# Kernel optimization log

Measured on AMD Instinct MI355X. Metric: run time of the kernel, lower is better.

## Reference

```python
import jax, jax.numpy as jnp
import numpy as np

NUM_HEADS = 16
HEAD_DIM = 64
ROPE_BASE = 10000.0


def _rope_cos_sin(seq_len, head_dim, dtype):
    inv_freq = 1.0 / (ROPE_BASE ** (jnp.arange(0, head_dim, 2, dtype=jnp.float32) / head_dim))
    t = jnp.arange(seq_len, dtype=jnp.float32)
    freqs = t[:, None] * inv_freq[None, :]          # (S, head_dim/2)
    emb = jnp.concatenate([freqs, freqs], axis=-1)  # (S, head_dim)
    return jnp.cos(emb).astype(dtype), jnp.sin(emb).astype(dtype)


def _rotate_half(x):
    x1, x2 = jnp.split(x, 2, axis=-1)
    return jnp.concatenate([-x2, x1], axis=-1)


def setup_inputs() -> dict:
    key = jax.random.key(0)
    k1, k2, k3 = jax.random.split(key, 3)
    B, S, D = 2, 2048, 1024
    x = jax.random.normal(k1, (B, S, D), dtype=jnp.float32)
    Wq = jax.random.normal(k2, (D, D), dtype=jnp.float32) * (D ** -0.5)
    Wkv = jax.random.normal(k3, (2 * D, D), dtype=jnp.float32) * (D ** -0.5)
    mask = jnp.tril(jnp.ones((S, S), dtype=jnp.int32))  # causal mask
    return {"x": x, "Wq": Wq, "Wkv": Wkv, "mask": mask}


def reference(x, Wq, Wkv, mask):
    B, S, D = x.shape
    H, Hd = NUM_HEADS, HEAD_DIM

    # projections (torch Linear: x @ W.T)
    q = (x @ Wq.T).reshape(B, S, H, Hd).transpose(0, 2, 1, 3)           # (B,H,S,Hd)
    kv = (x @ Wkv.T).reshape(B, S, H, Hd, 2).transpose(0, 2, 1, 3, 4)   # (B,H,S,Hd,2)
    k = kv[..., 0]
    v = kv[..., 1]

    # RoPE
    cos, sin = _rope_cos_sin(S, Hd, x.dtype)  # (S,Hd) broadcast over (B,H)
    q = q * cos + _rotate_half(q) * sin
    k = k * cos + _rotate_half(k) * sin

    # attention with full score materialization (faithful to source)
    scale = 1.0 / jnp.sqrt(jnp.asarray(Hd, dtype=x.dtype))
    scores = jnp.einsum('bhqd,bhkd->bhqk', q, k) * scale                # (B,H,S,S)
    scores = jnp.where(mask == 0, -jnp.inf, scores)
    attn = jax.nn.softmax(scores, axis=-1)
    out = jnp.einsum('bhqk,bhkd->bhqd', attn, v)                        # (B,H,S,Hd)
    return out.transpose(0, 2, 1, 3).reshape(B, S, D)
```

## Files before the change

kernel.cpp:

```cpp
#include <hip/hip_runtime.h>
#include <hip/hip_bf16.h>
#include <math.h>


typedef short bfrag __attribute__((ext_vector_type(8)));
typedef float f32x4 __attribute__((ext_vector_type(4)));

__device__ __forceinline__ float bf2f(ushort u) {
    union { uint i; float f; } v; v.i = ((uint)u) << 16; return v.f;
}
__device__ __forceinline__ ushort f2bf(float f) {
    union { uint i; float f; } v; v.f = f;
    uint u = v.i;
    return (ushort)((u + 0x7fffu + ((u >> 16) & 1u)) >> 16);
}

#define MFMA16 __builtin_amdgcn_mfma_f32_16x16x32_bf16

__device__ __forceinline__ void gl_lds16(const ushort* g, ushort* l) {
    __builtin_amdgcn_global_load_lds(
        (const __attribute__((address_space(1))) void*)g,
        (__attribute__((address_space(3))) void*)l, 16, 0, 0);
}

__global__ __launch_bounds__(256)
void cvt_bf16(const float* __restrict__ x, const float* __restrict__ wq,
              const float* __restrict__ wkv, ushort* __restrict__ xb,
              ushort* __restrict__ wb)
{
    const size_t NX = 4096u * 1024u, NWQ = 1024u * 1024u;
    size_t i8 = ((size_t)blockIdx.x * 256 + threadIdx.x) * 8;
    const float* src;
    ushort* dst;
    if (i8 < NX) { src = x + i8; dst = xb + i8; }
    else {
        size_t j = i8 - NX;
        dst = wb + j;
        src = (j < NWQ) ? (wq + j) : (wkv + (j - NWQ));
    }
    float4 a = *(const float4*)(src);
    float4 c = *(const float4*)(src + 4);
    ushort u[8];
    u[0] = f2bf(a.x); u[1] = f2bf(a.y); u[2] = f2bf(a.z); u[3] = f2bf(a.w);
    u[4] = f2bf(c.x); u[5] = f2bf(c.y); u[6] = f2bf(c.z); u[7] = f2bf(c.w);
    *(uint4*)dst = *(uint4*)u;
}

__global__ __launch_bounds__(256)
void rope_table(float2* __restrict__ tab)
{
    int t  = blockIdx.x * 256 + threadIdx.x;
    int fi = t & 31, s = t >> 5;
    float invf = (float)exp((double)fi * -0.28782313662425574);
    float thf  = (float)s * invf;
    const double TWO_PI = 6.283185307179586476925287;
    double th = (double)thf;
    double kq = __builtin_rint(th * (1.0 / TWO_PI));
    float r = (float)(th - kq * TWO_PI);
    tab[t] = make_float2(cosf(r), sinf(r));
}

__global__ __launch_bounds__(256)
void gemm_qkv(const ushort* __restrict__ xb, const ushort* __restrict__ wb,
              const float2* __restrict__ tab, ushort* __restrict__ Qb,
              ushort* __restrict__ Kb, ushort* __restrict__ Vt)
{
    __shared__ ushort Ash[128][64];
    __shared__ ushort Bsh[128][64];

    const int tid  = threadIdx.x;
    const int lane = tid & 63, wv = tid >> 6;
    const int quad = lane >> 4, li = lane & 15;
    const int m0 = blockIdx.x * 128, n0 = blockIdx.y * 128;

    f32x4 acc[2][8];
#pragma unroll
    for (int mi = 0; mi < 2; mi++)
#pragma unroll
        for (int j = 0; j < 8; j++) acc[mi][j] = (f32x4){0.f, 0.f, 0.f, 0.f};

    const int r8  = lane >> 3;
    const int gch = ((lane & 7) ^ r8) * 8;
    const ushort* gA = xb + (size_t)(m0 + wv * 32 + r8) * 1024 + gch;
    const ushort* gB = wb + (size_t)(n0 + wv * 32 + r8) * 1024 + gch;

    for (int k0 = 0; k0 < 1024; k0 += 64) {
        __syncthreads();
#pragma unroll
        for (int c = 0; c < 4; c++) {
            gl_lds16(gA + (size_t)(c * 8) * 1024 + k0, &Ash[wv * 32 + c * 8][0]);
            gl_lds16(gB + (size_t)(c * 8) * 1024 + k0, &Bsh[wv * 32 + c * 8][0]);
        }
        __syncthreads();

        const int sw = li & 7;
#pragma unroll
        for (int ks = 0; ks < 2; ks++) {
            bfrag af[2], bf[8];
#pragma unroll
            for (int mi = 0; mi < 2; mi++)
                af[mi] = *(const bfrag*)
                    &Ash[wv * 32 + mi * 16 + li][(((ks << 2) | quad) ^ sw) * 8];
#pragma unroll
            for (int j = 0; j < 8; j++)
                bf[j] = *(const bfrag*)
                    &Bsh[j * 16 + li][(((ks << 2) | quad) ^ sw) * 8];
#pragma unroll
            for (int mi = 0; mi < 2; mi++)
#pragma unroll
                for (int j = 0; j < 8; j++)
                    acc[mi][j] = MFMA16(af[mi], bf[j], acc[mi][j], 0, 0, 0);
        }
    }

    if (n0 < 1024) {
        const int hbase = n0 >> 6;
#pragma unroll
        for (int mi = 0; mi < 2; mi++)
#pragma unroll
            for (int r = 0; r < 4; r++) {
                int m = m0 + wv * 32 + mi * 16 + quad * 4 + r;
                int bb = m >> 11, s = m & 2047;
                float2 t0 = tab[s * 32 + li];
                float2 t1 = tab[s * 32 + li + 16];
#pragma unroll
                for (int j = 0; j < 8; j++) {
                    float v  = acc[mi][j][r];
                    float vp = acc[mi][j ^ 2][r];
                    float2 tt = (j & 1) ? t1 : t0;
                    float rh = (j & 2) ? vp : -vp;
                    int h = hbase + (j >> 2), hd = (j & 3) * 16 + li;
                    Qb[(size_t)((bb * 16 + h) * 2048 + s) * 64 + hd] =
                        f2bf(v * tt.x + rh * tt.y);
                }
            }
    } else {
        const int h = (n0 - 1024) >> 7;
        const int li2 = li >> 1;
        if ((li & 1) == 0) {
#pragma unroll
            for (int mi = 0; mi < 2; mi++)
#pragma unroll
                for (int r = 0; r < 4; r++) {
                    int m = m0 + wv * 32 + mi * 16 + quad * 4 + r;
                    int bb = m >> 11, s = m & 2047;
                    float2 tt4[4];
#pragma unroll
                    for (int jj = 0; jj < 4; jj++)
                        tt4[jj] = tab[s * 32 + jj * 8 + li2];
#pragma unroll
                    for (int j = 0; j < 8; j++) {
                        float v  = acc[mi][j][r];
                        float vp = acc[mi][j ^ 4][r];
                        float2 tt = tt4[j & 3];
                        float rh = (j & 4) ? vp : -vp;
                        int hd = j * 8 + li2;
                        Kb[(size_t)((bb * 16 + h) * 2048 + s) * 64 + hd] =
                            f2bf(v * tt.x + rh * tt.y);
                    }
                }
        } else {
#pragma unroll
            for (int mi = 0; mi < 2; mi++) {
                int m4 = m0 + wv * 32 + mi * 16 + quad * 4;
                int bb = m4 >> 11, s0 = m4 & 2047;
#pragma unroll
                for (int j = 0; j < 8; j++) {
                    int hd = j * 8 + li2;
                    ushort u4[4];
#pragma unroll
                    for (int r = 0; r < 4; r++) u4[r] = f2bf(acc[mi][j][r]);
                    *(ushort4*)&Vt[(size_t)((bb * 16 + h) * 64 + hd) * 2048 + s0] =
                        *(ushort4*)u4;
                }
            }
        }
    }
}

__global__ __launch_bounds__(256)
void attn(const ushort* __restrict__ Qb, const ushort* __restrict__ Kb,
          const ushort* __restrict__ Vt, float* __restrict__ out)
{
    __shared__ ushort Ksh[64][72];
    __shared__ ushort Vsh[64][72];
    __shared__ ushort Psh[4][16][72];

    const int tid  = threadIdx.x;
    const int lane = tid & 63, w = tid >> 6;
    const int quad = lane >> 4, li = lane & 15;
    const int qt = ((31 - (int)blockIdx.x) + (int)blockIdx.y) & 31;
    const int bh = blockIdx.y;
    const int b = bh >> 4, h = bh & 15;

    const int qrow = qt * 64 + w * 16 + li;
    const ushort* qp = Qb + (size_t)(bh * 2048 + qrow) * 64;
    bfrag qa0 = *(const bfrag*)(qp + quad * 8);
    bfrag qa1 = *(const bfrag*)(qp + quad * 8 + 32);

    f32x4 o[4];
#pragma unroll
    for (int j = 0; j < 4; j++) o[j] = (f32x4){0.f, 0.f, 0.f, 0.f};
    float lrow = 0.f;

    const int srow = tid >> 2, sc0 = (tid & 3) * 16;
    const ushort* kbase = Kb + (size_t)bh * 2048 * 64;
    const ushort* vbase = Vt + (size_t)bh * 64 * 2048;

    uint4 ka, kb_, va, vb_;
    {
        const ushort* gk = kbase + (size_t)srow * 64 + sc0;
        ka  = *(const uint4*)gk;
        kb_ = *(const uint4*)(gk + 8);
        const ushort* gv = vbase + (size_t)srow * 2048 + sc0;
        va  = *(const uint4*)gv;
        vb_ = *(const uint4*)(gv + 8);
    }

    const float C = 0.125f * 1.4426950408889634f;

    for (int kt = 0; kt <= qt; ++kt) {
        __syncthreads();
        *(uint4*)&Ksh[srow][sc0]     = ka;
        *(uint4*)&Ksh[srow][sc0 + 8] = kb_;
        *(uint4*)&Vsh[srow][sc0]     = va;
        *(uint4*)&Vsh[srow][sc0 + 8] = vb_;
        __syncthreads();

        if (kt < qt) {
            const ushort* gk = kbase + (size_t)((kt + 1) * 64 + srow) * 64 + sc0;
            ka  = *(const uint4*)gk;
            kb_ = *(const uint4*)(gk + 8);
            const ushort* gv = vbase + (size_t)srow * 2048 + (kt + 1) * 64 + sc0;
            va  = *(const uint4*)gv;
            vb_ = *(const uint4*)(gv + 8);
        }

        f32x4 sc[4];
        __builtin_amdgcn_s_setprio(1);
#pragma unroll
        for (int j = 0; j < 4; j++) {
            bfrag kb0 = *(const bfrag*)&Ksh[j * 16 + li][quad * 8];
            bfrag kb1 = *(const bfrag*)&Ksh[j * 16 + li][quad * 8 + 32];
            f32x4 z = (f32x4){0.f, 0.f, 0.f, 0.f};
            z = MFMA16(kb0, qa0, z, 0, 0, 0);
            z = MFMA16(kb1, qa1, z, 0, 0, 0);
            sc[j] = z;
        }
        __builtin_amdgcn_s_setprio(0);

        if (kt == qt) {
#pragma unroll
            for (int j = 0; j < 4; j++) {
                int kg0 = kt * 64 + j * 16 + quad * 4;
#pragma unroll
                for (int r = 0; r < 4; r++)
                    sc[j][r] = (kg0 + r <= qrow) ? sc[j][r] : -3.0e38f;
            }
        }

        float rs = 0.f;
#pragma unroll
        for (int j = 0; j < 4; j++) {
            ushort pk[4];
#pragma unroll
            for (int r = 0; r < 4; r++) {
                float pv = exp2f(sc[j][r] * C);
                uint pu = __float_as_uint(pv);
                pk[r] = (ushort)(pu >> 16);
                rs += __uint_as_float(pu & 0xffff0000u);
            }
            *(ushort4*)&Psh[w][li][j * 16 + quad * 4] = *(ushort4*)pk;
        }
        rs += __shfl_xor(rs, 16);
        rs += __shfl_xor(rs, 32);
        lrow += rs;

        asm volatile("s_waitcnt lgkmcnt(0)" ::: "memory");
        bfrag pa0 = *(const bfrag*)&Psh[w][li][quad * 8];
        bfrag pa1 = *(const bfrag*)&Psh[w][li][quad * 8 + 32];

        __builtin_amdgcn_s_setprio(1);
#pragma unroll
        for (int j = 0; j < 4; j++) {
            bfrag vb0 = *(const bfrag*)&Vsh[j * 16 + li][quad * 8];
            bfrag vb1 = *(const bfrag*)&Vsh[j * 16 + li][quad * 8 + 32];
            o[j] = MFMA16(pa0, vb0, o[j], 0, 0, 0);
            o[j] = MFMA16(pa1, vb1, o[j], 0, 0, 0);
        }
        __builtin_amdgcn_s_setprio(0);
    }

    float lf[4];
#pragma unroll
    for (int r = 0; r < 4; r++)
        lf[r] = __shfl(lrow, (lane & 48) + quad * 4 + r);

#pragma unroll
    for (int j = 0; j < 4; j++)
#pragma unroll
        for (int r = 0; r < 4; r++) {
            int s = qt * 64 + w * 16 + quad * 4 + r;
            out[(size_t)(b * 2048 + s) * 1024 + h * 64 + j * 16 + li] =
                o[j][r] / lf[r];
        }
}

extern "C" void kernel_launch(void* const* d_in, const int* in_sizes, int n_in,
                              void* d_out, int out_size, void* d_ws, size_t ws_size,
                              hipStream_t stream)
{
    (void)in_sizes; (void)n_in; (void)out_size; (void)ws_size;
    const float* x   = (const float*)d_in[0];
    const float* wq  = (const float*)d_in[1];
    const float* wkv = (const float*)d_in[2];

    ushort* xb = (ushort*)d_ws;
    ushort* wb = xb + (size_t)4096 * 1024;
    float2* tab = (float2*)(wb + (size_t)3072 * 1024);
    ushort* Qb = (ushort*)(tab + 65536);
    ushort* Kb = Qb + (size_t)2 * 16 * 2048 * 64;
    ushort* Vt = Kb + (size_t)2 * 16 * 2048 * 64;
    float* out = (float*)d_out;

    cvt_bf16<<<3584, 256, 0, stream>>>(x, wq, wkv, xb, wb);
    rope_table<<<256, 256, 0, stream>>>(tab);
    dim3 g1(32, 24);
    gemm_qkv<<<g1, 256, 0, stream>>>(xb, wb, tab, Qb, Kb, Vt);
    dim3 g4(32, 32);
    attn<<<g4, 256, 0, stream>>>(Qb, Kb, Vt, out);
}
```

Baseline: 182.3 us.

## Merge rope table into convert kernel, preload V fragments, round P properly

The RoPE table kernel is folded into the bf16 conversion kernel as extra blocks, which removes one launch. In the attention loop, all V fragments are loaded from LDS into registers right after the barrier, before the next tile's global prefetch, so the LDS reads can overlap the QK and softmax work. The P conversion now uses hardware round-to-nearest bf16 and sums the unrounded fp32 probabilities instead of the truncated ones. This changes numerics slightly and raises register pressure from the eight held V fragments.

```diff
diff --git a/kernel.cpp b/kernel.cpp
--- a/kernel.cpp
+++ b/kernel.cpp
@@ -14,6 +14,11 @@
     uint u = v.i;
     return (ushort)((u + 0x7fffu + ((u >> 16) & 1u)) >> 16);
 }
+__device__ __forceinline__ ushort f2bf_hw(float f) {
+    union { __hip_bfloat16 b; ushort u; } cv;
+    cv.b = __float2bfloat16(f);
+    return cv.u;
+}
 
 #define MFMA16 __builtin_amdgcn_mfma_f32_16x16x32_bf16
 
@@ -24,10 +29,22 @@
 }
 
 __global__ __launch_bounds__(256)
-void cvt_bf16(const float* __restrict__ x, const float* __restrict__ wq,
+void cvt_rope(const float* __restrict__ x, const float* __restrict__ wq,
               const float* __restrict__ wkv, ushort* __restrict__ xb,
-              ushort* __restrict__ wb)
+              ushort* __restrict__ wb, float2* __restrict__ tab)
 {
+    if (blockIdx.x >= 3584) {
+        int t  = ((int)blockIdx.x - 3584) * 256 + threadIdx.x;
+        int fi = t & 31, s = t >> 5;
+        float invf = (float)exp((double)fi * -0.28782313662425574);
+        float thf  = (float)s * invf;
+        const double TWO_PI = 6.283185307179586476925287;
+        double th = (double)thf;
+        double kq = __builtin_rint(th * (1.0 / TWO_PI));
+        float r = (float)(th - kq * TWO_PI);
+        tab[t] = make_float2(cosf(r), sinf(r));
+        return;
+    }
     const size_t NX = 4096u * 1024u, NWQ = 1024u * 1024u;
     size_t i8 = ((size_t)blockIdx.x * 256 + threadIdx.x) * 8;
     const float* src;
@@ -44,20 +61,6 @@
     u[0] = f2bf(a.x); u[1] = f2bf(a.y); u[2] = f2bf(a.z); u[3] = f2bf(a.w);
     u[4] = f2bf(c.x); u[5] = f2bf(c.y); u[6] = f2bf(c.z); u[7] = f2bf(c.w);
     *(uint4*)dst = *(uint4*)u;
-}
-
-__global__ __launch_bounds__(256)
-void rope_table(float2* __restrict__ tab)
-{
-    int t  = blockIdx.x * 256 + threadIdx.x;
-    int fi = t & 31, s = t >> 5;
-    float invf = (float)exp((double)fi * -0.28782313662425574);
-    float thf  = (float)s * invf;
-    const double TWO_PI = 6.283185307179586476925287;
-    double th = (double)thf;
-    double kq = __builtin_rint(th * (1.0 / TWO_PI));
-    float r = (float)(th - kq * TWO_PI);
-    tab[t] = make_float2(cosf(r), sinf(r));
 }
 
 __global__ __launch_bounds__(256)
@@ -227,6 +230,13 @@
         *(uint4*)&Vsh[srow][sc0 + 8] = vb_;
         __syncthreads();
 
+        bfrag vf[8];
+#pragma unroll
+        for (int j = 0; j < 4; j++) {
+            vf[2 * j]     = *(const bfrag*)&Vsh[j * 16 + li][quad * 8];
+            vf[2 * j + 1] = *(const bfrag*)&Vsh[j * 16 + li][quad * 8 + 32];
+        }
+
         if (kt < qt) {
             const ushort* gk = kbase + (size_t)((kt + 1) * 64 + srow) * 64 + sc0;
             ka  = *(const uint4*)gk;
@@ -266,9 +276,8 @@
 #pragma unroll
             for (int r = 0; r < 4; r++) {
                 float pv = exp2f(sc[j][r] * C);
-                uint pu = __float_as_uint(pv);
-                pk[r] = (ushort)(pu >> 16);
-                rs += __uint_as_float(pu & 0xffff0000u);
+                rs += pv;
+                pk[r] = f2bf_hw(pv);
             }
             *(ushort4*)&Psh[w][li][j * 16 + quad * 4] = *(ushort4*)pk;
         }
@@ -283,10 +292,8 @@
         __builtin_amdgcn_s_setprio(1);
 #pragma unroll
         for (int j = 0; j < 4; j++) {
-            bfrag vb0 = *(const bfrag*)&Vsh[j * 16 + li][quad * 8];
-            bfrag vb1 = *(const bfrag*)&Vsh[j * 16 + li][quad * 8 + 32];
-            o[j] = MFMA16(pa0, vb0, o[j], 0, 0, 0);
-            o[j] = MFMA16(pa1, vb1, o[j], 0, 0, 0);
+            o[j] = MFMA16(pa0, vf[2 * j],     o[j], 0, 0, 0);
+            o[j] = MFMA16(pa1, vf[2 * j + 1], o[j], 0, 0, 0);
         }
         __builtin_amdgcn_s_setprio(0);
     }
@@ -323,8 +330,7 @@
     ushort* Vt = Kb + (size_t)2 * 16 * 2048 * 64;
     float* out = (float*)d_out;
 
-    cvt_bf16<<<3584, 256, 0, stream>>>(x, wq, wkv, xb, wb);
-    rope_table<<<256, 256, 0, stream>>>(tab);
+    cvt_rope<<<3840, 256, 0, stream>>>(x, wq, wkv, xb, wb, tab);
     dim3 g1(32, 24);
     gemm_qkv<<<g1, 256, 0, stream>>>(xb, wb, tab, Qb, Kb, Vt);
     dim3 g4(32, 32);
```

After: 185.3 us. No clear change (+1.7%).
